# Optimization experiments

Hardware: AMD Instinct MI355X
Metric: run time of the kernel (lower is better)

## Reference

```python
import jax, jax.numpy as jnp
import numpy as np

TOKENS, IN_F, OUT_F = 8192, 4096, 4096

def setup_inputs() -> dict:
    key = jax.random.key(0)
    k1, k2, k3, k4 = jax.random.split(key, 4)
    x = jax.random.randint(k1, (TOKENS, IN_F), -128, 128, dtype=jnp.int32).astype(jnp.int8)
    weight = jax.random.randint(k2, (OUT_F, IN_F), -128, 128, dtype=jnp.int32).astype(jnp.int8)
    # per-output-channel static dequant scale (small positive values, as for int8 quant)
    dequant_scale = (jax.random.uniform(k3, (OUT_F,), dtype=jnp.float32) * 0.01 + 1e-4)
    bias = (jax.random.normal(k4, (OUT_F,), dtype=jnp.float32) * 0.02).astype(jnp.float16)
    return {"x": x, "weight": weight, "dequant_scale": dequant_scale, "bias": bias}

def reference(x, weight, dequant_scale, bias):
    acc = jnp.matmul(x.astype(jnp.int32), weight.T.astype(jnp.int32))
    # fused epilogue: per-channel dequant + bias add, cast to fp16 output
    out = (acc.astype(jnp.float32) * dequant_scale[None, :]
           + bias.astype(jnp.float32)[None, :]).astype(jnp.float16)
    # module's forward returns (output, bias)
    return (out, bias)
```

## Files before the change

kernel.cpp:

```cpp
#include <hip/hip_runtime.h>
#include <hip/hip_fp16.h>

#define TOKENS 8192
#define IN_F   4096
#define OUT_F  4096

typedef __attribute__((ext_vector_type(4))) int i32x4;

__global__ void pack_i8_kernel(const int4* __restrict__ src, int4* __restrict__ dst, int n16) {
    int stride = gridDim.x * blockDim.x;
    for (int i = blockIdx.x * blockDim.x + threadIdx.x; i < n16; i += stride) {
        int4 a = src[4 * i + 0];
        int4 b = src[4 * i + 1];
        int4 c = src[4 * i + 2];
        int4 d = src[4 * i + 3];
        int4 o;
        o.x = (int)((a.x & 0xffu) | ((a.y & 0xffu) << 8) | ((a.z & 0xffu) << 16) | ((a.w & 0xffu) << 24));
        o.y = (int)((b.x & 0xffu) | ((b.y & 0xffu) << 8) | ((b.z & 0xffu) << 16) | ((b.w & 0xffu) << 24));
        o.z = (int)((c.x & 0xffu) | ((c.y & 0xffu) << 8) | ((c.z & 0xffu) << 16) | ((c.w & 0xffu) << 24));
        o.w = (int)((d.x & 0xffu) | ((d.y & 0xffu) << 8) | ((d.z & 0xffu) << 16) | ((d.w & 0xffu) << 24));
        dst[i] = o;
    }
}

__global__ void bias_echo_kernel(const float* __restrict__ bias, float* __restrict__ out_tail) {
    int i = blockIdx.x * blockDim.x + threadIdx.x;
    if (i < OUT_F) out_tail[i] = bias[i];
}

__global__ __launch_bounds__(256, 2) void gemm_i8_kernel(
    const char* __restrict__ A,
    const char* __restrict__ B,
    const float* __restrict__ scale,
    const float* __restrict__ bias,
    float* __restrict__ out)
{
    __shared__ char lds[2][2][16384];

    const int tid  = threadIdx.x;
    const int wid  = tid >> 6;
    const int lane = tid & 63;

    const int nwg = gridDim.x;
    const int bid = blockIdx.x;
    const int swz = (bid & 7) * (nwg >> 3) + (bid >> 3);
    const int tm = swz >> 5;
    const int tn = swz & 31;

    const char* ag = A + (size_t)(tm * 128) * IN_F;
    const char* bg = B + (size_t)(tn * 128) * IN_F;

    const int srow   = lane >> 3;
    const int schunk = (lane & 7) ^ srow;

    i32x4 acc[4][4];
#pragma unroll
    for (int m = 0; m < 4; ++m)
#pragma unroll
        for (int n = 0; n < 4; ++n)
            acc[m][n] = (i32x4){0, 0, 0, 0};

#define STAGE(buf, kt)                                                                     \
    do {                                                                                   \
        const char* abase = ag + (kt) * 128;                                               \
        const char* bbase = bg + (kt) * 128;                                               \
        _Pragma("unroll")                                                                  \
        for (int j = 0; j < 4; ++j) {                                                      \
            int q = wid * 4 + j;                                                           \
            size_t go = (size_t)(q * 8 + srow) * IN_F + schunk * 16;                       \
            __builtin_amdgcn_global_load_lds(                                              \
                (const __attribute__((address_space(1))) void*)(abase + go),               \
                (__attribute__((address_space(3))) void*)(&lds[buf][0][q * 1024]),         \
                16, 0, 0);                                                                 \
            __builtin_amdgcn_global_load_lds(                                              \
                (const __attribute__((address_space(1))) void*)(bbase + go),               \
                (__attribute__((address_space(3))) void*)(&lds[buf][1][q * 1024]),         \
                16, 0, 0);                                                                 \
        }                                                                                  \
    } while (0)

    const int rA  = ((wid >> 1) * 64 + (lane & 15)) * 128;
    const int rB  = ((wid & 1) * 64 + (lane & 15)) * 128;
    const int sw0 = ((lane >> 4) ^ (lane & 7)) << 4;

#define COMPUTE(buf)                                                                       \
    do {                                                                                   \
        const char* al = &lds[buf][0][0];                                                  \
        const char* bl = &lds[buf][1][0];                                                  \
        i32x4 afr[2][4], bfr[2][4];                                                        \
        _Pragma("unroll")                                                                  \
        for (int kk = 0; kk < 2; ++kk) {                                                   \
            const int sw = sw0 ^ (kk << 6);                                                \
            _Pragma("unroll")                                                              \
            for (int m = 0; m < 4; ++m)                                                    \
                afr[kk][m] = *(const i32x4*)(al + rA + m * 2048 + sw);                     \
            _Pragma("unroll")                                                              \
            for (int n = 0; n < 4; ++n)                                                    \
                bfr[kk][n] = *(const i32x4*)(bl + rB + n * 2048 + sw);                     \
        }                                                                                  \
        _Pragma("unroll")                                                                  \
        for (int kk = 0; kk < 2; ++kk)                                                     \
            _Pragma("unroll")                                                              \
            for (int m = 0; m < 4; ++m)                                                    \
                _Pragma("unroll")                                                          \
                for (int n = 0; n < 4; ++n)                                                \
                    acc[m][n] = __builtin_amdgcn_mfma_i32_16x16x64_i8(                     \
                        afr[kk][m], bfr[kk][n], acc[m][n], 0, 0, 0);                       \
    } while (0)

    STAGE(0, 0);
    __syncthreads();

    int cur = 0;
    const int NKT = IN_F / 128;
    for (int kt = 0; kt < NKT; ++kt) {
        if (kt < NKT - 1) {
            if (cur == 0) STAGE(1, kt + 1); else STAGE(0, kt + 1);
        }
        if (cur == 0) COMPUTE(0); else COMPUTE(1);
        __syncthreads();
        cur ^= 1;
    }

    const int fbase = tn * 128 + (wid & 1) * 64 + (lane & 15);
    const int tbase = tm * 128 + (wid >> 1) * 64 + ((lane >> 4) << 2);
    float sc[4], bi[4];
#pragma unroll
    for (int n = 0; n < 4; ++n) {
        sc[n] = scale[fbase + n * 16];
        bi[n] = bias[fbase + n * 16];
    }
#pragma unroll
    for (int m = 0; m < 4; ++m)
#pragma unroll
        for (int n = 0; n < 4; ++n)
#pragma unroll
            for (int r = 0; r < 4; ++r) {
                int t = tbase + m * 16 + r;
                float v = (float)acc[m][n][r] * sc[n] + bi[n];
                out[(size_t)t * OUT_F + fbase + n * 16] = (float)__float2half_rn(v);
            }
#undef STAGE
#undef COMPUTE
}

extern "C" void kernel_launch(void* const* d_in, const int* in_sizes, int n_in,
                              void* d_out, int out_size, void* d_ws, size_t ws_size,
                              hipStream_t stream) {
    const int*   x_i32 = (const int*)d_in[0];
    const int*   w_i32 = (const int*)d_in[1];
    const float* scale = (const float*)d_in[2];
    const float* bias  = (const float*)d_in[3];
    float*       out   = (float*)d_out;

    char* xp = (char*)d_ws;
    char* wp = xp + (size_t)TOKENS * IN_F;

    pack_i8_kernel<<<2048, 256, 0, stream>>>((const int4*)x_i32, (int4*)xp, TOKENS * IN_F / 16);
    pack_i8_kernel<<<1024, 256, 0, stream>>>((const int4*)w_i32, (int4*)wp, OUT_F * IN_F / 16);

    gemm_i8_kernel<<<(TOKENS / 128) * (OUT_F / 128), 256, 0, stream>>>(xp, wp, scale, bias, out);

    bias_echo_kernel<<<(OUT_F + 255) / 256, 256, 0, stream>>>(bias, out + (size_t)TOKENS * OUT_F);
}
```

Baseline: 201.2 us.

## Enlarge GEMM tile to 256x256 with 4-stage LDS pipeline and fuse prep kernels

The GEMM moves from 128x128 tiles with 4 waves to 256x256 tiles with 8 waves, and the K step drops to 64. Loads go through a 4-deep ring of LDS buffers, with explicit vmcnt waits and raw barriers so global loads for later stages overlap the MFMAs. MFMA sections run at raised s_setprio. The two pack kernels and the bias echo are merged into one prep launch to cut launch overhead. LDS use grows to 128KB per block, which limits occupancy, and the larger accumulator array raises register pressure.

```diff
diff --git a/kernel.cpp b/kernel.cpp
--- a/kernel.cpp
+++ b/kernel.cpp
@@ -4,144 +4,145 @@
 #define TOKENS 8192
 #define IN_F   4096
 #define OUT_F  4096
+#define NKT    (IN_F / 64)
 
 typedef __attribute__((ext_vector_type(4))) int i32x4;
 
-__global__ void pack_i8_kernel(const int4* __restrict__ src, int4* __restrict__ dst, int n16) {
-    int stride = gridDim.x * blockDim.x;
-    for (int i = blockIdx.x * blockDim.x + threadIdx.x; i < n16; i += stride) {
-        int4 a = src[4 * i + 0];
-        int4 b = src[4 * i + 1];
-        int4 c = src[4 * i + 2];
-        int4 d = src[4 * i + 3];
+__global__ void prep_kernel(const int4* __restrict__ xs, const int4* __restrict__ ws,
+                            const float* __restrict__ bias,
+                            int4* __restrict__ xp, int4* __restrict__ wp,
+                            float* __restrict__ out_tail) {
+    const int NX = TOKENS * IN_F / 16;
+    const int NW = OUT_F * IN_F / 16;
+    const int gid = blockIdx.x * blockDim.x + threadIdx.x;
+    const int stride = gridDim.x * blockDim.x;
+    for (int i = gid; i < NX + NW; i += stride) {
+        const int4* s; int4* d; int j;
+        if (i < NX) { s = xs; d = xp; j = i; }
+        else        { s = ws; d = wp; j = i - NX; }
+        int4 a = s[4 * j + 0];
+        int4 b = s[4 * j + 1];
+        int4 c = s[4 * j + 2];
+        int4 e = s[4 * j + 3];
         int4 o;
         o.x = (int)((a.x & 0xffu) | ((a.y & 0xffu) << 8) | ((a.z & 0xffu) << 16) | ((a.w & 0xffu) << 24));
         o.y = (int)((b.x & 0xffu) | ((b.y & 0xffu) << 8) | ((b.z & 0xffu) << 16) | ((b.w & 0xffu) << 24));
         o.z = (int)((c.x & 0xffu) | ((c.y & 0xffu) << 8) | ((c.z & 0xffu) << 16) | ((c.w & 0xffu) << 24));
-        o.w = (int)((d.x & 0xffu) | ((d.y & 0xffu) << 8) | ((d.z & 0xffu) << 16) | ((d.w & 0xffu) << 24));
-        dst[i] = o;
+        o.w = (int)((e.x & 0xffu) | ((e.y & 0xffu) << 8) | ((e.z & 0xffu) << 16) | ((e.w & 0xffu) << 24));
+        d[j] = o;
     }
+    if (gid < OUT_F) out_tail[gid] = bias[gid];
 }
 
-__global__ void bias_echo_kernel(const float* __restrict__ bias, float* __restrict__ out_tail) {
-    int i = blockIdx.x * blockDim.x + threadIdx.x;
-    if (i < OUT_F) out_tail[i] = bias[i];
-}
-
-__global__ __launch_bounds__(256, 2) void gemm_i8_kernel(
+__global__ __launch_bounds__(512, 2) void gemm_i8_kernel(
     const char* __restrict__ A,
     const char* __restrict__ B,
     const float* __restrict__ scale,
     const float* __restrict__ bias,
     float* __restrict__ out)
 {
-    __shared__ char lds[2][2][16384];
+    __shared__ char lds[4][2][16384];
 
     const int tid  = threadIdx.x;
     const int wid  = tid >> 6;
     const int lane = tid & 63;
+    const int wm   = wid >> 2;
+    const int wn   = wid & 3;
 
     const int nwg = gridDim.x;
     const int bid = blockIdx.x;
     const int swz = (bid & 7) * (nwg >> 3) + (bid >> 3);
-    const int tm = swz >> 5;
-    const int tn = swz & 31;
+    const int tm = swz >> 4;
+    const int tn = swz & 15;
 
-    const char* ag = A + (size_t)(tm * 128) * IN_F;
-    const char* bg = B + (size_t)(tn * 128) * IN_F;
+    const char* ag = A + (size_t)(tm * 256) * IN_F;
+    const char* bg = B + (size_t)(tn * 256) * IN_F;
 
-    const int srow   = lane >> 3;
-    const int schunk = (lane & 7) ^ srow;
+    const int srow16 = wid * 16 + (lane >> 2);
+    const int schunk = ((lane & 3) ^ ((lane >> 2) & 3)) << 4;
+    const int ldst   = wid * 1024 + lane * 16;
 
-    i32x4 acc[4][4];
+    i32x4 acc[8][4];
 #pragma unroll
-    for (int m = 0; m < 4; ++m)
+    for (int m = 0; m < 8; ++m)
 #pragma unroll
         for (int n = 0; n < 4; ++n)
             acc[m][n] = (i32x4){0, 0, 0, 0};
 
-#define STAGE(buf, kt)                                                                     \
+#define STAGE(r, t)                                                                        \
     do {                                                                                   \
-        const char* abase = ag + (kt) * 128;                                               \
-        const char* bbase = bg + (kt) * 128;                                               \
         _Pragma("unroll")                                                                  \
-        for (int j = 0; j < 4; ++j) {                                                      \
-            int q = wid * 4 + j;                                                           \
-            size_t go = (size_t)(q * 8 + srow) * IN_F + schunk * 16;                       \
+        for (int j = 0; j < 2; ++j) {                                                      \
+            size_t go = (size_t)(j * 128 + srow16) * IN_F + (size_t)(t) * 64 + schunk;     \
             __builtin_amdgcn_global_load_lds(                                              \
-                (const __attribute__((address_space(1))) void*)(abase + go),               \
-                (__attribute__((address_space(3))) void*)(&lds[buf][0][q * 1024]),         \
+                (const __attribute__((address_space(1))) void*)(ag + go),                  \
+                (__attribute__((address_space(3))) void*)(&lds[r][0][j * 8192 + ldst]),    \
                 16, 0, 0);                                                                 \
             __builtin_amdgcn_global_load_lds(                                              \
-                (const __attribute__((address_space(1))) void*)(bbase + go),               \
-                (__attribute__((address_space(3))) void*)(&lds[buf][1][q * 1024]),         \
+                (const __attribute__((address_space(1))) void*)(bg + go),                  \
+                (__attribute__((address_space(3))) void*)(&lds[r][1][j * 8192 + ldst]),    \
                 16, 0, 0);                                                                 \
         }                                                                                  \
     } while (0)
 
-    const int rA  = ((wid >> 1) * 64 + (lane & 15)) * 128;
-    const int rB  = ((wid & 1) * 64 + (lane & 15)) * 128;
-    const int sw0 = ((lane >> 4) ^ (lane & 7)) << 4;
+    const int kg   = lane >> 4;
+    const int sxa  = lane & 3;
+    const int aoff = (wm * 128 + (lane & 15)) * 64 + ((kg ^ sxa) << 4);
+    const int boff = (wn * 64  + (lane & 15)) * 64 + ((kg ^ sxa) << 4);
 
-#define COMPUTE(buf)                                                                       \
+#define STEP(t, VM, DOSTAGE)                                                               \
     do {                                                                                   \
-        const char* al = &lds[buf][0][0];                                                  \
-        const char* bl = &lds[buf][1][0];                                                  \
-        i32x4 afr[2][4], bfr[2][4];                                                        \
+        asm volatile("s_waitcnt vmcnt(" #VM ")" ::: "memory");                             \
+        __builtin_amdgcn_s_barrier();                                                      \
+        asm volatile("" ::: "memory");                                                     \
+        __builtin_amdgcn_sched_barrier(0);                                                 \
+        if (DOSTAGE) STAGE(((t) + 3) & 3, (t) + 3);                                        \
+        const char* al = &lds[(t) & 3][0][0];                                              \
+        const char* bl = &lds[(t) & 3][1][0];                                              \
+        i32x4 afr[8], bfr[4];                                                              \
         _Pragma("unroll")                                                                  \
-        for (int kk = 0; kk < 2; ++kk) {                                                   \
-            const int sw = sw0 ^ (kk << 6);                                                \
-            _Pragma("unroll")                                                              \
-            for (int m = 0; m < 4; ++m)                                                    \
-                afr[kk][m] = *(const i32x4*)(al + rA + m * 2048 + sw);                     \
+        for (int m = 0; m < 8; ++m) afr[m] = *(const i32x4*)(al + aoff + m * 1024);        \
+        _Pragma("unroll")                                                                  \
+        for (int n = 0; n < 4; ++n) bfr[n] = *(const i32x4*)(bl + boff + n * 1024);        \
+        __builtin_amdgcn_s_setprio(1);                                                     \
+        _Pragma("unroll")                                                                  \
+        for (int m = 0; m < 8; ++m)                                                        \
             _Pragma("unroll")                                                              \
             for (int n = 0; n < 4; ++n)                                                    \
-                bfr[kk][n] = *(const i32x4*)(bl + rB + n * 2048 + sw);                     \
-        }                                                                                  \
-        _Pragma("unroll")                                                                  \
-        for (int kk = 0; kk < 2; ++kk)                                                     \
-            _Pragma("unroll")                                                              \
-            for (int m = 0; m < 4; ++m)                                                    \
-                _Pragma("unroll")                                                          \
-                for (int n = 0; n < 4; ++n)                                                \
-                    acc[m][n] = __builtin_amdgcn_mfma_i32_16x16x64_i8(                     \
-                        afr[kk][m], bfr[kk][n], acc[m][n], 0, 0, 0);                       \
+                acc[m][n] = __builtin_amdgcn_mfma_i32_16x16x64_i8(                         \
+                    afr[m], bfr[n], acc[m][n], 0, 0, 0);                                   \
+        __builtin_amdgcn_s_setprio(0);                                                     \
     } while (0)
 
     STAGE(0, 0);
-    __syncthreads();
+    STAGE(1, 1);
+    STAGE(2, 2);
 
-    int cur = 0;
-    const int NKT = IN_F / 128;
-    for (int kt = 0; kt < NKT; ++kt) {
-        if (kt < NKT - 1) {
-            if (cur == 0) STAGE(1, kt + 1); else STAGE(0, kt + 1);
-        }
-        if (cur == 0) COMPUTE(0); else COMPUTE(1);
-        __syncthreads();
-        cur ^= 1;
-    }
+    for (int t = 0; t < NKT - 3; ++t) STEP(t, 8, 1);
+    STEP(NKT - 3, 8, 0);
+    STEP(NKT - 2, 4, 0);
+    STEP(NKT - 1, 0, 0);
 
-    const int fbase = tn * 128 + (wid & 1) * 64 + (lane & 15);
-    const int tbase = tm * 128 + (wid >> 1) * 64 + ((lane >> 4) << 2);
+    const int col  = tn * 256 + wn * 64 + (lane & 15);
+    const int row0 = tm * 256 + wm * 128 + ((lane >> 4) << 2);
     float sc[4], bi[4];
 #pragma unroll
     for (int n = 0; n < 4; ++n) {
-        sc[n] = scale[fbase + n * 16];
-        bi[n] = bias[fbase + n * 16];
+        sc[n] = scale[col + n * 16];
+        bi[n] = bias[col + n * 16];
     }
 #pragma unroll
-    for (int m = 0; m < 4; ++m)
+    for (int m = 0; m < 8; ++m)
 #pragma unroll
         for (int n = 0; n < 4; ++n)
 #pragma unroll
             for (int r = 0; r < 4; ++r) {
-                int t = tbase + m * 16 + r;
                 float v = (float)acc[m][n][r] * sc[n] + bi[n];
-                out[(size_t)t * OUT_F + fbase + n * 16] = (float)__float2half_rn(v);
+                out[(size_t)(row0 + m * 16 + r) * OUT_F + col + n * 16] =
+                    (float)__float2half_rn(v);
             }
 #undef STAGE
-#undef COMPUTE
+#undef STEP
 }
 
 extern "C" void kernel_launch(void* const* d_in, const int* in_sizes, int n_in,
@@ -156,10 +157,8 @@
     char* xp = (char*)d_ws;
     char* wp = xp + (size_t)TOKENS * IN_F;
 
-    pack_i8_kernel<<<2048, 256, 0, stream>>>((const int4*)x_i32, (int4*)xp, TOKENS * IN_F / 16);
-    pack_i8_kernel<<<1024, 256, 0, stream>>>((const int4*)w_i32, (int4*)wp, OUT_F * IN_F / 16);
+    prep_kernel<<<3072, 256, 0, stream>>>((const int4*)x_i32, (const int4*)w_i32, bias,
+                                          (int4*)xp, (int4*)wp, out + (size_t)TOKENS * OUT_F);
 
-    gemm_i8_kernel<<<(TOKENS / 128) * (OUT_F / 128), 256, 0, stream>>>(xp, wp, scale, bias, out);
-
-    bias_echo_kernel<<<(OUT_F + 255) / 256, 256, 0, stream>>>(bias, out + (size_t)TOKENS * OUT_F);
+    gemm_i8_kernel<<<(TOKENS / 256) * (OUT_F / 256), 512, 0, stream>>>(xp, wp, scale, bias, out);
 }
```

Result: faster. 192.0 us (-4.6%).
